# Performance work log

Hardware: AMD Instinct MI355X
Metric: run time of the kernel (lower is better)

## Reference

```python
import jax, jax.numpy as jnp
import numpy as np

B, C, D, H, W = 2, 64, 20, 20, 20
RATIO = 8
CQ = C // RATIO  # Q/K channels = 8


def setup_inputs() -> dict:
    key = jax.random.key(0)
    ks = jax.random.split(key, 8)
    s = 0.05
    return {
        "x": jax.random.normal(ks[0], (B, C, D, H, W), dtype=jnp.float32),
        "Wq": jax.random.normal(ks[1], (CQ, C), dtype=jnp.float32) * s,
        "bq": jax.random.normal(ks[2], (CQ,), dtype=jnp.float32) * s,
        "Wk": jax.random.normal(ks[3], (CQ, C), dtype=jnp.float32) * s,
        "bk": jax.random.normal(ks[4], (CQ,), dtype=jnp.float32) * s,
        "Wv": jax.random.normal(ks[5], (C, C), dtype=jnp.float32) * s,
        "bv": jax.random.normal(ks[6], (C,), dtype=jnp.float32) * s,
        "gamma": jax.random.normal(ks[7], (1,), dtype=jnp.float32) * s,
    }


def reference(x, Wq, bq, Wk, bk, Wv, bv, gamma):
    b, c, *spatial = x.shape
    n = int(np.prod(spatial))
    xf = x.reshape(b, c, n)  # [B, C, N]
    # 1x1 convs == per-position channel matmuls
    Q = jnp.einsum('oc,bcn->bon', Wq, xf) + bq[None, :, None]  # [B, Cq, N]
    K = jnp.einsum('oc,bcn->bon', Wk, xf) + bk[None, :, None]  # [B, Cq, N]
    V = jnp.einsum('oc,bcn->bon', Wv, xf) + bv[None, :, None]  # [B, C, N]
    # energy[b, n, m] = sum_q Q[b, q, n] * K[b, q, m]  (no scaling, as in source)
    energy = jnp.einsum('bqn,bqm->bnm', Q, K)  # [B, N, N]
    attention = jax.nn.softmax(energy, axis=-1)
    # out[b, c, n] = sum_m V[b, c, m] * attention[b, n, m]
    out = jnp.einsum('bcm,bnm->bcn', V, attention)
    out = out.reshape(b, c, *spatial)
    return gamma * out + x
```

## Files before the change

### kernel.cpp

```cpp
#include <hip/hip_runtime.h>
#include <hip/hip_bf16.h>

#define BB 2
#define CC 64
#define CQk 8
#define NN 8000
#define TB 256
#define QT 4

using f32x4  = __attribute__((ext_vector_type(4))) float;
using bf16x8 = __attribute__((ext_vector_type(8))) short;
typedef unsigned long long ull;
typedef unsigned short ushort_t;

__device__ __forceinline__ ushort_t f2bf(float f) {
    __hip_bfloat16 h = __float2bfloat16(f);
    return *reinterpret_cast<ushort_t*>(&h);
}

__global__ void detect_dtype(const void* __restrict__ x, int* __restrict__ flag)
{
    const float* xf = (const float*)x;
    const int t = threadIdx.x;
    const float a = fabsf(xf[t * 8]);
    const int ok = (a > 9.765625e-4f && a < 16.0f) ? 1 : 0;
    const unsigned long long m = __ballot(ok);
    if (t == 0) flag[0] = (__popcll(m) >= 48) ? 1 : 0;
}

__device__ __forceinline__ float loadF(const void* p, size_t i, int isf) {
    return isf ? ((const float*)p)[i]
               : __bfloat162float(((const __hip_bfloat16*)p)[i]);
}

__device__ __forceinline__ int vidx(int n) {
    const int h = (n & 15) >> 2;
    const int i = (n & 3) + (((n >> 4) & 1) << 2);
    return (n & ~31) + h * 8 + i;
}

__global__ __launch_bounds__(TB) void qkv_kernel(
    const void* __restrict__ x,
    const void* __restrict__ Wq, const void* __restrict__ bq,
    const void* __restrict__ Wk, const void* __restrict__ bk,
    const void* __restrict__ Wv, const void* __restrict__ bv,
    ushort_t* __restrict__ Qbf, ushort_t* __restrict__ Kbf,
    ushort_t* __restrict__ Vtp, const int* __restrict__ flag)
{
    __shared__ float sW[16][CC];
    __shared__ float sB[16];
    const int isf = flag[0];
    const int t = threadIdx.x;
    const int chunk = blockIdx.y;

    for (int i = t; i < 16 * CC; i += TB) {
        const int rr = i >> 6, c = i & 63;
        const int r = chunk * 16 + rr;
        float w;
        if (r < CQk)          w = loadF(Wq, (size_t)r * CC + c, isf);
        else if (r < 2 * CQk) w = loadF(Wk, (size_t)(r - CQk) * CC + c, isf);
        else                  w = loadF(Wv, (size_t)(r - 2 * CQk) * CC + c, isf);
        sW[rr][c] = w;
    }
    if (t < 16) {
        const int r = chunk * 16 + t;
        float bias;
        if (r < CQk)          bias = loadF(bq, r, isf);
        else if (r < 2 * CQk) bias = loadF(bk, r - CQk, isf);
        else                  bias = loadF(bv, r - 2 * CQk, isf);
        sB[t] = bias;
    }
    __syncthreads();

    const int pos = blockIdx.x * TB + t;
    if (pos >= BB * NN) return;
    const int b = pos / NN, n = pos % NN;

    float xv[CC];
    const size_t xbase = (size_t)b * CC * NN + n;
#pragma unroll
    for (int c = 0; c < CC; ++c) xv[c] = loadF(x, xbase + (size_t)c * NN, isf);

    float acc[16];
#pragma unroll
    for (int rr = 0; rr < 16; ++rr) {
        float a = sB[rr];
#pragma unroll
        for (int c = 0; c < CC; ++c) a += sW[rr][c] * xv[c];
        acc[rr] = a;
    }

    const size_t pn = (size_t)b * NN + n;
    if (chunk == 0) {
        bf16x8 pq, pk;
#pragma unroll
        for (int j = 0; j < 8; ++j) {
            pq[j] = (short)f2bf(acc[j]);
            pk[j] = (short)f2bf(acc[8 + j]);
        }
        *(bf16x8*)&Qbf[pn * 8] = pq;
        *(bf16x8*)&Kbf[pn * 8] = pk;
    } else {
        const int c0 = (chunk - 1) * 16;
        const int vn = vidx(n);
#pragma unroll
        for (int rr = 0; rr < 16; ++rr)
            Vtp[((size_t)b * CC + c0 + rr) * NN + vn] = f2bf(acc[rr]);
    }
}

__global__ __launch_bounds__(64) void attn_mfma(
    const ushort_t* __restrict__ Qbf, const ushort_t* __restrict__ Kbf,
    const ushort_t* __restrict__ Vtp,
    float* __restrict__ O, float* __restrict__ L, const int MS)
{
    __shared__ __align__(16) ushort_t sP[QT][32 * 16];

    const int lane = threadIdx.x;
    const int cl = lane & 15, h = lane >> 4;
    const int q0 = blockIdx.x * (QT * 16);
    const int s = blockIdx.y, b = blockIdx.z;
    const int S = gridDim.y;
    const int mBeg = s * MS, mEnd = mBeg + MS;
    const size_t bN = (size_t)b * NN;

    bf16x8 qa[QT];
#pragma unroll
    for (int t = 0; t < QT; ++t) {
        bf16x8 z;
#pragma unroll
        for (int j = 0; j < 8; ++j) z[j] = 0;
        if (h == 0) z = *(const bf16x8*)&Qbf[(bN + q0 + t * 16 + cl) * 8];
        qa[t] = z;
    }

    bf16x8 ones;
#pragma unroll
    for (int j = 0; j < 8; ++j) ones[j] = (short)0x3F80;

    const f32x4 zf = {0.f, 0.f, 0.f, 0.f};
    f32x4 acc[QT][4];
    f32x4 lac[QT];
#pragma unroll
    for (int t = 0; t < QT; ++t) {
        lac[t] = zf;
#pragma unroll
        for (int ct = 0; ct < 4; ++ct) acc[t][ct] = zf;
    }

    for (int m0 = mBeg; m0 < mEnd; m0 += 32) {
        const bool tail = (mEnd - m0) < 32;

        bf16x8 kb0, kb1;
#pragma unroll
        for (int j = 0; j < 8; ++j) { kb0[j] = 0; kb1[j] = 0; }
        if (h == 0) {
            kb0 = *(const bf16x8*)&Kbf[(bN + m0 + cl) * 8];
            if (!tail) kb1 = *(const bf16x8*)&Kbf[(bN + m0 + 16 + cl) * 8];
        }

        bf16x8 vb[4];
#pragma unroll
        for (int ct = 0; ct < 4; ++ct) {
            bf16x8 v = *(const bf16x8*)&Vtp[((size_t)b * CC + ct * 16 + cl) * NN + m0 + h * 8];
            if (tail) { v[4] = 0; v[5] = 0; v[6] = 0; v[7] = 0; }
            vb[ct] = v;
        }

#pragma unroll
        for (int t = 0; t < QT; ++t) {
            f32x4 e0 = __builtin_amdgcn_mfma_f32_16x16x32_bf16(qa[t], kb0, zf, 0, 0, 0);
            f32x4 e1 = __builtin_amdgcn_mfma_f32_16x16x32_bf16(qa[t], kb1, zf, 0, 0, 0);
            ull u0 = 0, u1 = 0;
#pragma unroll
            for (int r = 0; r < 4; ++r) {
                const ull p0 = (ull)f2bf(__expf(e0[r]));
                const ull p1 = tail ? 0ull : (ull)f2bf(__expf(e1[r]));
                u0 |= p0 << (16 * r);
                u1 |= p1 << (16 * r);
            }
            char* base = (char*)&sP[t][0];
            *(ull*)(base + cl * 32 + h * 8)       = u0;
            *(ull*)(base + 512 + cl * 32 + h * 8) = u1;
        }

        ull pa0[QT], pa1[QT];
#pragma unroll
        for (int t = 0; t < QT; ++t) {
            unsigned addr = (unsigned)(uintptr_t)&sP[t][0] + (unsigned)(cl * 2 + h * 128);
            asm volatile("ds_read_b64_tr_b16 %0, %1 offset:0"
                         : "=v"(pa0[t]) : "v"(addr) : "memory");
            asm volatile("ds_read_b64_tr_b16 %0, %1 offset:512"
                         : "=v"(pa1[t]) : "v"(addr) : "memory");
        }
        asm volatile("s_waitcnt lgkmcnt(0)" ::: "memory");
        __builtin_amdgcn_sched_barrier(0);

#pragma unroll
        for (int t = 0; t < QT; ++t) {
            bf16x8 af;
#pragma unroll
            for (int j = 0; j < 4; ++j) {
                af[j]     = (short)(ushort_t)(pa0[t] >> (16 * j));
                af[4 + j] = (short)(ushort_t)(pa1[t] >> (16 * j));
            }
#pragma unroll
            for (int ct = 0; ct < 4; ++ct)
                acc[t][ct] = __builtin_amdgcn_mfma_f32_16x16x32_bf16(af, vb[ct], acc[t][ct], 0, 0, 0);
            lac[t] = __builtin_amdgcn_mfma_f32_16x16x32_bf16(af, ones, lac[t], 0, 0, 0);
        }
    }

    const size_t obase = ((size_t)b * S + s) * NN;
#pragma unroll
    for (int t = 0; t < QT; ++t) {
#pragma unroll
        for (int ct = 0; ct < 4; ++ct) {
#pragma unroll
            for (int r = 0; r < 4; ++r)
                O[(obase + q0 + t * 16 + 4 * h + r) * CC + ct * 16 + cl] = acc[t][ct][r];
        }
        if (cl == 0) {
#pragma unroll
            for (int r = 0; r < 4; ++r)
                L[obase + q0 + t * 16 + 4 * h + r] = lac[t][r];
        }
    }
}

__global__ __launch_bounds__(TB) void reduce_write(
    const float* __restrict__ O, const float* __restrict__ L,
    const void* __restrict__ x, const void* __restrict__ gamma,
    void* __restrict__ out, const int S, const int* __restrict__ flag)
{
    __shared__ float sO[64][65];
    const int isf = flag[0];
    const int t = threadIdx.x;
    const int n0 = blockIdx.x * 64;
    const int b = blockIdx.y;
    const float g = loadF(gamma, 0, isf);

    {
        const int c = t & 63, nl = t >> 6;
        for (int nn = nl; nn < 64; nn += 4) {
            const int n = n0 + nn;
            float acc = 0.f, lsum = 0.f;
            for (int si = 0; si < S; ++si) {
                acc  += O[(((size_t)b * S + si) * NN + n) * CC + c];
                lsum += L[((size_t)b * S + si) * NN + n];
            }
            sO[nn][c] = g * (acc / lsum);
        }
    }
    __syncthreads();
    {
        const int nn = t & 63, cb = t >> 6;
        const int n = n0 + nn;
#pragma unroll
        for (int ci = 0; ci < 16; ++ci) {
            const int c = cb * 16 + ci;
            const size_t idx = ((size_t)b * CC + c) * NN + n;
            const float val = sO[nn][c] + loadF(x, idx, isf);
            if (isf) ((float*)out)[idx] = val;
            else     ((__hip_bfloat16*)out)[idx] = __float2bfloat16(val);
        }
    }
}

extern "C" void kernel_launch(void* const* d_in, const int* in_sizes, int n_in,
                              void* d_out, int out_size, void* d_ws, size_t ws_size,
                              hipStream_t stream)
{
    const void* x     = d_in[0];
    const void* Wq    = d_in[1];
    const void* bq    = d_in[2];
    const void* Wk    = d_in[3];
    const void* bk    = d_in[4];
    const void* Wv    = d_in[5];
    const void* bv    = d_in[6];
    const void* gamma = d_in[7];

    char* base = (char*)d_ws;
    int* flag = (int*)base;
    size_t off = 256;
    ushort_t* Qbf = (ushort_t*)(base + off); off += (size_t)BB * NN * CQk * 2;
    ushort_t* Kbf = (ushort_t*)(base + off); off += (size_t)BB * NN * CQk * 2;
    ushort_t* Vtp = (ushort_t*)(base + off); off += ((size_t)BB * CC * NN + 64) * 2;
    off = (off + 255) & ~(size_t)255;

    int S = 4;
    while (S > 1 && off + (size_t)BB * S * NN * (CC + 1) * 4 > ws_size) S >>= 1;
    const int MS = NN / S;
    float* Obuf = (float*)(base + off);
    float* Lbuf = Obuf + (size_t)BB * S * NN * CC;

    detect_dtype<<<1, 64, 0, stream>>>(x, flag);

    dim3 g1((BB * NN + TB - 1) / TB, 5);
    qkv_kernel<<<g1, TB, 0, stream>>>(x, Wq, bq, Wk, bk, Wv, bv, Qbf, Kbf, Vtp, flag);

    dim3 g2(NN / (QT * 16), S, BB);
    attn_mfma<<<g2, 64, 0, stream>>>(Qbf, Kbf, Vtp, Obuf, Lbuf, MS);

    dim3 g3(NN / 64, BB);
    reduce_write<<<g3, TB, 0, stream>>>(Obuf, Lbuf, x, gamma, d_out, S, flag);
}
```

Baseline: 123.3 us.

## Fuse attention split-K and reduction into one 8-wave block with LDS combine

Replaces the single-wave split-KV attention kernel and its separate global-memory reduction kernel with one 512-thread block per 64 queries. Eight waves stride over key blocks, then combine partial outputs and row sums through LDS atomics before applying normalisation, gamma and the residual in the same kernel. It also computes the energy tile transposed (K as A operand), so the exponentiated probabilities land directly in MFMA A-operand layout, removing the LDS transpose round trip. Q is prescaled by log2(e) so exp2f can replace __expf. This trades the global O/L buffers and an extra launch for LDS atomics, a block-wide sync, and a grid of only 250 blocks.

```diff
diff --git a/kernel.cpp b/kernel.cpp
--- a/kernel.cpp
+++ b/kernel.cpp
@@ -7,10 +7,11 @@
 #define NN 8000
 #define TB 256
 #define QT 4
+#define NWAVE 8
+#define NBLK32 250
 
 using f32x4  = __attribute__((ext_vector_type(4))) float;
 using bf16x8 = __attribute__((ext_vector_type(8))) short;
-typedef unsigned long long ull;
 typedef unsigned short ushort_t;
 
 __device__ __forceinline__ ushort_t f2bf(float f) {
@@ -95,7 +96,7 @@
         bf16x8 pq, pk;
 #pragma unroll
         for (int j = 0; j < 8; ++j) {
-            pq[j] = (short)f2bf(acc[j]);
+            pq[j] = (short)f2bf(acc[j] * 1.44269504089f);
             pk[j] = (short)f2bf(acc[8 + j]);
         }
         *(bf16x8*)&Qbf[pn * 8] = pq;
@@ -109,29 +110,35 @@
     }
 }
 
-__global__ __launch_bounds__(64) void attn_mfma(
+__global__ __launch_bounds__(512) void attn_fused(
     const ushort_t* __restrict__ Qbf, const ushort_t* __restrict__ Kbf,
     const ushort_t* __restrict__ Vtp,
-    float* __restrict__ O, float* __restrict__ L, const int MS)
-{
-    __shared__ __align__(16) ushort_t sP[QT][32 * 16];
-
-    const int lane = threadIdx.x;
+    const void* __restrict__ x, const void* __restrict__ gamma,
+    void* __restrict__ out, const int* __restrict__ flag)
+{
+    __shared__ float sO[64][65];
+    __shared__ float sL[64];
+    const int isf = flag[0];
+    const int tid = threadIdx.x;
+    const int lane = tid & 63;
+    const int w = tid >> 6;
     const int cl = lane & 15, h = lane >> 4;
-    const int q0 = blockIdx.x * (QT * 16);
-    const int s = blockIdx.y, b = blockIdx.z;
-    const int S = gridDim.y;
-    const int mBeg = s * MS, mEnd = mBeg + MS;
+    const int q0 = blockIdx.x * 64;
+    const int b = blockIdx.y;
     const size_t bN = (size_t)b * NN;
 
-    bf16x8 qa[QT];
+    for (int i = tid; i < 64 * 65; i += 512) (&sO[0][0])[i] = 0.f;
+    if (tid < 64) sL[tid] = 0.f;
+    __syncthreads();
+
+    bf16x8 qb[QT];
 #pragma unroll
     for (int t = 0; t < QT; ++t) {
         bf16x8 z;
 #pragma unroll
         for (int j = 0; j < 8; ++j) z[j] = 0;
         if (h == 0) z = *(const bf16x8*)&Qbf[(bN + q0 + t * 16 + cl) * 8];
-        qa[t] = z;
+        qb[t] = z;
     }
 
     bf16x8 ones;
@@ -148,61 +155,31 @@
         for (int ct = 0; ct < 4; ++ct) acc[t][ct] = zf;
     }
 
-    for (int m0 = mBeg; m0 < mEnd; m0 += 32) {
-        const bool tail = (mEnd - m0) < 32;
-
-        bf16x8 kb0, kb1;
-#pragma unroll
-        for (int j = 0; j < 8; ++j) { kb0[j] = 0; kb1[j] = 0; }
+    for (int bi = w; bi < NBLK32; bi += NWAVE) {
+        const int m0 = bi * 32;
+
+        bf16x8 ka0, ka1;
+#pragma unroll
+        for (int j = 0; j < 8; ++j) { ka0[j] = 0; ka1[j] = 0; }
         if (h == 0) {
-            kb0 = *(const bf16x8*)&Kbf[(bN + m0 + cl) * 8];
-            if (!tail) kb1 = *(const bf16x8*)&Kbf[(bN + m0 + 16 + cl) * 8];
+            ka0 = *(const bf16x8*)&Kbf[(bN + m0 + cl) * 8];
+            ka1 = *(const bf16x8*)&Kbf[(bN + m0 + 16 + cl) * 8];
         }
 
         bf16x8 vb[4];
 #pragma unroll
-        for (int ct = 0; ct < 4; ++ct) {
-            bf16x8 v = *(const bf16x8*)&Vtp[((size_t)b * CC + ct * 16 + cl) * NN + m0 + h * 8];
-            if (tail) { v[4] = 0; v[5] = 0; v[6] = 0; v[7] = 0; }
-            vb[ct] = v;
-        }
+        for (int ct = 0; ct < 4; ++ct)
+            vb[ct] = *(const bf16x8*)&Vtp[((size_t)b * CC + ct * 16 + cl) * NN + m0 + h * 8];
 
 #pragma unroll
         for (int t = 0; t < QT; ++t) {
-            f32x4 e0 = __builtin_amdgcn_mfma_f32_16x16x32_bf16(qa[t], kb0, zf, 0, 0, 0);
-            f32x4 e1 = __builtin_amdgcn_mfma_f32_16x16x32_bf16(qa[t], kb1, zf, 0, 0, 0);
-            ull u0 = 0, u1 = 0;
+            f32x4 e0 = __builtin_amdgcn_mfma_f32_16x16x32_bf16(ka0, qb[t], zf, 0, 0, 0);
+            f32x4 e1 = __builtin_amdgcn_mfma_f32_16x16x32_bf16(ka1, qb[t], zf, 0, 0, 0);
+            bf16x8 af;
 #pragma unroll
             for (int r = 0; r < 4; ++r) {
-                const ull p0 = (ull)f2bf(__expf(e0[r]));
-                const ull p1 = tail ? 0ull : (ull)f2bf(__expf(e1[r]));
-                u0 |= p0 << (16 * r);
-                u1 |= p1 << (16 * r);
-            }
-            char* base = (char*)&sP[t][0];
-            *(ull*)(base + cl * 32 + h * 8)       = u0;
-            *(ull*)(base + 512 + cl * 32 + h * 8) = u1;
-        }
-
-        ull pa0[QT], pa1[QT];
-#pragma unroll
-        for (int t = 0; t < QT; ++t) {
-            unsigned addr = (unsigned)(uintptr_t)&sP[t][0] + (unsigned)(cl * 2 + h * 128);
-            asm volatile("ds_read_b64_tr_b16 %0, %1 offset:0"
-                         : "=v"(pa0[t]) : "v"(addr) : "memory");
-            asm volatile("ds_read_b64_tr_b16 %0, %1 offset:512"
-                         : "=v"(pa1[t]) : "v"(addr) : "memory");
-        }
-        asm volatile("s_waitcnt lgkmcnt(0)" ::: "memory");
-        __builtin_amdgcn_sched_barrier(0);
-
-#pragma unroll
-        for (int t = 0; t < QT; ++t) {
-            bf16x8 af;
-#pragma unroll
-            for (int j = 0; j < 4; ++j) {
-                af[j]     = (short)(ushort_t)(pa0[t] >> (16 * j));
-                af[4 + j] = (short)(ushort_t)(pa1[t] >> (16 * j));
+                af[r]     = (short)f2bf(exp2f(e0[r]));
+                af[4 + r] = (short)f2bf(exp2f(e1[r]));
             }
 #pragma unroll
             for (int ct = 0; ct < 4; ++ct)
@@ -211,59 +188,32 @@
         }
     }
 
-    const size_t obase = ((size_t)b * S + s) * NN;
 #pragma unroll
     for (int t = 0; t < QT; ++t) {
 #pragma unroll
-        for (int ct = 0; ct < 4; ++ct) {
+        for (int ct = 0; ct < 4; ++ct)
 #pragma unroll
             for (int r = 0; r < 4; ++r)
-                O[(obase + q0 + t * 16 + 4 * h + r) * CC + ct * 16 + cl] = acc[t][ct][r];
-        }
+                atomicAdd(&sO[t * 16 + 4 * h + r][ct * 16 + cl], acc[t][ct][r]);
         if (cl == 0) {
 #pragma unroll
             for (int r = 0; r < 4; ++r)
-                L[obase + q0 + t * 16 + 4 * h + r] = lac[t][r];
-        }
-    }
-}
-
-__global__ __launch_bounds__(TB) void reduce_write(
-    const float* __restrict__ O, const float* __restrict__ L,
-    const void* __restrict__ x, const void* __restrict__ gamma,
-    void* __restrict__ out, const int S, const int* __restrict__ flag)
-{
-    __shared__ float sO[64][65];
-    const int isf = flag[0];
-    const int t = threadIdx.x;
-    const int n0 = blockIdx.x * 64;
-    const int b = blockIdx.y;
+                atomicAdd(&sL[t * 16 + 4 * h + r], lac[t][r]);
+        }
+    }
+    __syncthreads();
+
     const float g = loadF(gamma, 0, isf);
-
-    {
-        const int c = t & 63, nl = t >> 6;
-        for (int nn = nl; nn < 64; nn += 4) {
-            const int n = n0 + nn;
-            float acc = 0.f, lsum = 0.f;
-            for (int si = 0; si < S; ++si) {
-                acc  += O[(((size_t)b * S + si) * NN + n) * CC + c];
-                lsum += L[((size_t)b * S + si) * NN + n];
-            }
-            sO[nn][c] = g * (acc / lsum);
-        }
-    }
-    __syncthreads();
-    {
-        const int nn = t & 63, cb = t >> 6;
-        const int n = n0 + nn;
-#pragma unroll
-        for (int ci = 0; ci < 16; ++ci) {
-            const int c = cb * 16 + ci;
-            const size_t idx = ((size_t)b * CC + c) * NN + n;
-            const float val = sO[nn][c] + loadF(x, idx, isf);
-            if (isf) ((float*)out)[idx] = val;
-            else     ((__hip_bfloat16*)out)[idx] = __float2bfloat16(val);
-        }
+    const int qq = tid & 63;
+    const int crow = tid >> 6;
+    const float rL = 1.0f / sL[qq];
+#pragma unroll
+    for (int p = 0; p < 8; ++p) {
+        const int c = p * 8 + crow;
+        const size_t idx = ((size_t)b * CC + c) * NN + q0 + qq;
+        const float val = g * sO[qq][c] * rL + loadF(x, idx, isf);
+        if (isf) ((float*)out)[idx] = val;
+        else     ((__hip_bfloat16*)out)[idx] = __float2bfloat16(val);
     }
 }
 
@@ -286,22 +236,12 @@
     ushort_t* Qbf = (ushort_t*)(base + off); off += (size_t)BB * NN * CQk * 2;
     ushort_t* Kbf = (ushort_t*)(base + off); off += (size_t)BB * NN * CQk * 2;
     ushort_t* Vtp = (ushort_t*)(base + off); off += ((size_t)BB * CC * NN + 64) * 2;
-    off = (off + 255) & ~(size_t)255;
-
-    int S = 4;
-    while (S > 1 && off + (size_t)BB * S * NN * (CC + 1) * 4 > ws_size) S >>= 1;
-    const int MS = NN / S;
-    float* Obuf = (float*)(base + off);
-    float* Lbuf = Obuf + (size_t)BB * S * NN * CC;
 
     detect_dtype<<<1, 64, 0, stream>>>(x, flag);
 
     dim3 g1((BB * NN + TB - 1) / TB, 5);
     qkv_kernel<<<g1, TB, 0, stream>>>(x, Wq, bq, Wk, bk, Wv, bv, Qbf, Kbf, Vtp, flag);
 
-    dim3 g2(NN / (QT * 16), S, BB);
-    attn_mfma<<<g2, 64, 0, stream>>>(Qbf, Kbf, Vtp, Obuf, Lbuf, MS);
-
-    dim3 g3(NN / 64, BB);
-    reduce_write<<<g3, TB, 0, stream>>>(Obuf, Lbuf, x, gamma, d_out, S, flag);
-}
+    dim3 g2(NN / 64, BB);
+    attn_fused<<<g2, 512, 0, stream>>>(Qbf, Kbf, Vtp, x, gamma, d_out, flag);
+}
```

Result: faster. 112.4 us (-8.8%).
